# Kernel optimization log

Hardware: AMD Instinct MI355X
Metric: run time of the kernel (lower is better)

The kernel has to match this reference:

```python
import jax, jax.numpy as jnp
import numpy as np

VOCAB, BLOCK, D, H, L = 50257, 2048, 768, 12, 4
B, T = 1, 2048
DH = D // H


def setup_inputs() -> dict:
    key = jax.random.key(0)
    ks = jax.random.split(key, 16)
    s = 0.02
    return {
        "tokens": jax.random.randint(ks[0], (B, T), 0, VOCAB),
        "wte": jax.random.normal(ks[1], (VOCAB, D), jnp.float32) * s,
        "wpe": jax.random.normal(ks[2], (BLOCK, D), jnp.float32) * s,
        "ln1_w": jnp.ones((L, D), jnp.float32),
        "ln1_b": jnp.zeros((L, D), jnp.float32),
        "qkv_w": jax.random.normal(ks[3], (L, D, 3 * D), jnp.float32) * s,
        "qkv_b": jnp.zeros((L, 3 * D), jnp.float32),
        "proj_w": jax.random.normal(ks[4], (L, D, D), jnp.float32) * s,
        "proj_b": jnp.zeros((L, D), jnp.float32),
        "ln2_w": jnp.ones((L, D), jnp.float32),
        "ln2_b": jnp.zeros((L, D), jnp.float32),
        "fc_w": jax.random.normal(ks[5], (L, D, 4 * D), jnp.float32) * s,
        "fc_b": jnp.zeros((L, 4 * D), jnp.float32),
        "fcp_w": jax.random.normal(ks[6], (L, 4 * D, D), jnp.float32) * s,
        "fcp_b": jnp.zeros((L, D), jnp.float32),
        "lnf_w": jnp.ones((D,), jnp.float32),
        "lnf_b": jnp.zeros((D,), jnp.float32),
    }


def _ln(x, w, b, eps=1e-5):
    m = jnp.mean(x, axis=-1, keepdims=True)
    v = jnp.mean((x - m) ** 2, axis=-1, keepdims=True)
    return (x - m) * jax.lax.rsqrt(v + eps) * w + b


def _attn(x, wq, bq, wp, bp):
    Bq, Tq, _ = x.shape
    qkv = x @ wq + bq  # [B,T,3D]
    q, k, v = jnp.split(qkv, 3, axis=-1)
    q = q.reshape(Bq, Tq, H, DH).transpose(0, 2, 1, 3)  # [B,H,T,dh]
    k = k.reshape(Bq, Tq, H, DH).transpose(0, 2, 1, 3)
    v = v.reshape(Bq, Tq, H, DH).transpose(0, 2, 1, 3)
    w = jnp.einsum("bhqd,bhkd->bhqk", q, k) / np.sqrt(DH).astype(np.float32)
    mask = jnp.tril(jnp.ones((Tq, Tq), bool))
    w = jnp.where(mask, w, -jnp.inf)
    w = jax.nn.softmax(w, axis=-1)
    y = jnp.einsum("bhqk,bhkd->bhqd", w, v)
    y = y.transpose(0, 2, 1, 3).reshape(Bq, Tq, D)
    return y @ wp + bp


def reference(tokens, wte, wpe, ln1_w, ln1_b, qkv_w, qkv_b, proj_w, proj_b,
              ln2_w, ln2_b, fc_w, fc_b, fcp_w, fcp_b, lnf_w, lnf_b):
    x = wte[tokens] + wpe[jnp.arange(tokens.shape[1])]  # [B,T,D]
    for l in range(L):
        x = x + _attn(_ln(x, ln1_w[l], ln1_b[l]), qkv_w[l], qkv_b[l], proj_w[l], proj_b[l])
        h = _ln(x, ln2_w[l], ln2_b[l]) @ fc_w[l] + fc_b[l]
        h = jax.nn.gelu(h, approximate=True)
        x = x + h @ fcp_w[l] + fcp_b[l]
    x = _ln(x, lnf_w, lnf_b)
    logits = x @ wte.T  # tied lm_head, [B,T,V]
    return logits
```

## Files before the change

kernel.cpp:

```cpp
#include <hip/hip_runtime.h>
#include <hip/hip_bf16.h>

#define TSEQ   2048
#define DMODEL 768
#define NHEAD  12
#define DHEAD  64
#define NLAYER 4
#define VOCAB  50257
#define VPAD   50304

typedef __attribute__((ext_vector_type(8))) short short8;
typedef __attribute__((ext_vector_type(4))) float f32x4;
typedef unsigned short ushort_t;

union F8 { short8 v; unsigned long long q[2]; };

__device__ __forceinline__ float b2f(ushort_t u) {
  return __uint_as_float(((unsigned)u) << 16);
}
__device__ __forceinline__ ushort_t f2bu(float f) {
  unsigned u = __float_as_uint(f);
  unsigned r = (u + 0x7fffu + ((u >> 16) & 1u)) >> 16;
  return (ushort_t)r;
}

__device__ __forceinline__ void gload_lds16(const void* g, void* l) {
  __builtin_amdgcn_global_load_lds(
      (const __attribute__((address_space(1))) unsigned int*)g,
      (__attribute__((address_space(3))) unsigned int*)l, 16, 0, 0);
}

__global__ __launch_bounds__(256) void embed_kernel(
    const int* __restrict__ tok, const float* __restrict__ wte,
    const float* __restrict__ wpe, float* __restrict__ x) {
  int i = blockIdx.x * 256 + threadIdx.x;
  int t = i / DMODEL;
  int d = i - t * DMODEL;
  x[i] = wte[tok[t] * DMODEL + d] + wpe[i];
}

__global__ __launch_bounds__(256) void cvt_kernel(
    const float* __restrict__ in, ushort_t* __restrict__ out, int n4) {
  for (int i = blockIdx.x * 256 + threadIdx.x; i < n4; i += gridDim.x * 256) {
    float4 f = reinterpret_cast<const float4*>(in)[i];
    ushort4 o;
    o.x = f2bu(f.x); o.y = f2bu(f.y); o.z = f2bu(f.z); o.w = f2bu(f.w);
    reinterpret_cast<ushort4*>(out)[i] = o;
  }
}

__global__ __launch_bounds__(256) void tcvt_kernel(
    const float* __restrict__ W, ushort_t* __restrict__ Wt, int K, int N) {
  __shared__ float Ts[32][33];
  int n0 = blockIdx.x * 32, k0 = blockIdx.y * 32;
  int tx = threadIdx.x & 31, ty = threadIdx.x >> 5;
#pragma unroll
  for (int s = 0; s < 4; ++s)
    Ts[ty + 8 * s][tx] = W[(size_t)(k0 + ty + 8 * s) * N + n0 + tx];
  __syncthreads();
#pragma unroll
  for (int s = 0; s < 4; ++s)
    Wt[(size_t)(n0 + ty + 8 * s) * K + k0 + tx] = f2bu(Ts[tx][ty + 8 * s]);
}

__global__ __launch_bounds__(256) void ln_kernel(
    const float* __restrict__ x, const float* __restrict__ w,
    const float* __restrict__ b, ushort_t* __restrict__ out) {
  int row = blockIdx.x;
  int t = threadIdx.x;
  const float* xr = x + row * DMODEL;
  float v0 = xr[t], v1 = xr[t + 256], v2 = xr[t + 512];
  float s = v0 + v1 + v2;
  float q = v0 * v0 + v1 * v1 + v2 * v2;
#pragma unroll
  for (int off = 32; off >= 1; off >>= 1) {
    s += __shfl_xor(s, off);
    q += __shfl_xor(q, off);
  }
  __shared__ float rs[4], rq[4];
  int wid = t >> 6;
  if ((t & 63) == 0) { rs[wid] = s; rq[wid] = q; }
  __syncthreads();
  s = rs[0] + rs[1] + rs[2] + rs[3];
  q = rq[0] + rq[1] + rq[2] + rq[3];
  float mean = s * (1.f / DMODEL);
  float var  = q * (1.f / DMODEL) - mean * mean;
  float rstd = rsqrtf(var + 1e-5f);
  ushort_t* o = out + row * DMODEL;
  o[t]       = f2bu((v0 - mean) * rstd * w[t]       + b[t]);
  o[t + 256] = f2bu((v1 - mean) * rstd * w[t + 256] + b[t + 256]);
  o[t + 512] = f2bu((v2 - mean) * rstd * w[t + 512] + b[t + 512]);
}

template <int TM, int TN, bool BIAS, bool RES, bool GELU, bool OUTBF16>
__global__ __launch_bounds__(256) void mm_kernel(
    const ushort_t* __restrict__ A, const ushort_t* __restrict__ Bt,
    const float* __restrict__ bias, const float* __restrict__ res,
    void* __restrict__ outp, int N, int K) {
  constexpr int HM = TM / 2, HN = TN / 2, FI = TM / 32, FJ = TN / 32;
  constexpr int NCA = TM / 64, NCB = TN / 64;
  __shared__ ushort_t Asm[TM * 32];
  __shared__ ushort_t Bsm[TN * 32];
  const int tid = threadIdx.x;
  const int lane = tid & 63, wid = tid >> 6;
  const int wr = wid >> 1, wc = wid & 1;
  const int l15 = lane & 15, c4 = lane >> 4;
  const int qc = c4 >> 1, e8 = (c4 & 1) * 8;
  const int rowA0 = blockIdx.y * TM, colB0 = blockIdx.x * TN;

  int aoff[FI], boff[FJ];
#pragma unroll
  for (int i = 0; i < FI; ++i) {
    int r = wr * HM + i * 16 + l15;
    aoff[i] = r * 64 + ((qc ^ ((r >> 1) & 3)) << 4) + e8;
  }
#pragma unroll
  for (int j = 0; j < FJ; ++j) {
    int r = wc * HN + j * 16 + l15;
    boff[j] = r * 64 + ((qc ^ ((r >> 1) & 3)) << 4) + e8;
  }
  const ushort_t* asrc[NCA]; ushort_t* adst[NCA];
  const ushort_t* bsrc[NCB]; ushort_t* bdst[NCB];
#pragma unroll
  for (int s = 0; s < NCA; ++s) {
    int ch = wid + s * 4;
    int r = ch * 16 + (lane >> 2);
    int q = (lane & 3) ^ ((r >> 1) & 3);
    asrc[s] = A + (size_t)(rowA0 + r) * K + q * 8;
    adst[s] = Asm + ch * 512;
  }
#pragma unroll
  for (int s = 0; s < NCB; ++s) {
    int ch = wid + s * 4;
    int r = ch * 16 + (lane >> 2);
    int q = (lane & 3) ^ ((r >> 1) & 3);
    bsrc[s] = Bt + (size_t)(colB0 + r) * K + q * 8;
    bdst[s] = Bsm + ch * 512;
  }

  f32x4 acc[FI][FJ] = {};
  const char* Ab = (const char*)Asm;
  const char* Bb = (const char*)Bsm;

  for (int kt = 0; kt < K; kt += 32) {
    __syncthreads();
#pragma unroll
    for (int s = 0; s < NCA; ++s) gload_lds16(asrc[s] + kt, adst[s]);
#pragma unroll
    for (int s = 0; s < NCB; ++s) gload_lds16(bsrc[s] + kt, bdst[s]);
    __syncthreads();
    short8 a[FI], b[FJ];
#pragma unroll
    for (int i = 0; i < FI; ++i) {
      F8 f;
      f.q[0] = *(const unsigned long long*)(Ab + aoff[i]);
      f.q[1] = *(const unsigned long long*)(Ab + (aoff[i] ^ 32));
      a[i] = f.v;
    }
#pragma unroll
    for (int j = 0; j < FJ; ++j) {
      F8 f;
      f.q[0] = *(const unsigned long long*)(Bb + boff[j]);
      f.q[1] = *(const unsigned long long*)(Bb + (boff[j] ^ 32));
      b[j] = f.v;
    }
#pragma unroll
    for (int i = 0; i < FI; ++i)
#pragma unroll
      for (int j = 0; j < FJ; ++j)
        acc[i][j] = __builtin_amdgcn_mfma_f32_16x16x32_bf16(a[i], b[j], acc[i][j], 0, 0, 0);
  }

#pragma unroll
  for (int i = 0; i < FI; ++i) {
    const int rbase = rowA0 + wr * HM + i * 16 + c4 * 4;
#pragma unroll
    for (int j = 0; j < FJ; ++j) {
      const int col = colB0 + wc * HN + j * 16 + l15;
      if (col < N) {
        float bv = BIAS ? bias[col] : 0.f;
#pragma unroll
        for (int t = 0; t < 4; ++t) {
          float v = acc[i][j][t] + bv;
          if (GELU) {
            float z = 1.5957691216057308f * (v + 0.044715f * v * v * v);
            float th = 1.f - 2.f / (__expf(z) + 1.f);
            v = 0.5f * v * (1.f + th);
          }
          size_t o = (size_t)(rbase + t) * N + col;
          if (RES)          ((float*)outp)[o] = v + res[o];
          else if (OUTBF16) ((ushort_t*)outp)[o] = f2bu(v);
          else              ((float*)outp)[o] = v;
        }
      }
    }
  }
}

__global__ __launch_bounds__(256) void fattn_kernel(
    const ushort_t* __restrict__ qkv, ushort_t* __restrict__ y) {
  const int id = blockIdx.x;
  const int w32 = id / NHEAD;
  const int h = id - w32 * NHEAD;
  const int qb = (w32 & 1) ? (w32 >> 1) : (31 - (w32 >> 1));
  const int q0 = qb * 64;

  __shared__ ushort_t Ksm[64 * 64];
  __shared__ ushort_t Vsm[64 * 64];
  __shared__ ushort_t Psm[4 * 16 * 64];

  const int tid = threadIdx.x;
  const int lane = tid & 63, wv = tid >> 6;
  const int l15 = lane & 15, c4 = lane >> 4;
  const int r7 = l15 & 7;

  const ushort_t* qrow = qkv + (size_t)(q0 + wv * 16 + l15) * (3 * DMODEL) + h * DHEAD;
  const short8 qf0 = *(const short8*)(qrow + c4 * 8);
  const short8 qf1 = *(const short8*)(qrow + 32 + c4 * 8);

  const ushort_t* ksrc[2]; ushort_t* kdst[2];
#pragma unroll
  for (int s = 0; s < 2; ++s) {
    int row = wv * 16 + s * 8 + (lane >> 3);
    int cs = (lane & 7) ^ (row & 7);
    ksrc[s] = qkv + (size_t)row * (3 * DMODEL) + DMODEL + h * DHEAD + cs * 8;
    kdst[s] = Ksm + ((wv * 2 + s) * 64) * 8;
  }
  const int vk = tid & 63, vd0 = (tid >> 6) * 8;
  const ushort_t* vsrc = qkv + (size_t)vk * (3 * DMODEL) + 2 * DMODEL + h * DHEAD;
  const int vkoff = ((vk >> 3) << 3) + (vk & 7);

  float m[4] = {-1e30f, -1e30f, -1e30f, -1e30f};
  float l[4] = {};
  f32x4 acc[4] = {};
  ushort_t* Pw = Psm + wv * 1024;

  for (int k0 = 0; k0 <= q0; k0 += 64) {
    const size_t koff = (size_t)k0 * (3 * DMODEL);
    short8 v0 = *(const short8*)(vsrc + koff + vd0);
    short8 v1 = *(const short8*)(vsrc + koff + vd0 + 32);
    __syncthreads();
#pragma unroll
    for (int s = 0; s < 2; ++s) gload_lds16(ksrc[s] + koff, kdst[s]);
#pragma unroll
    for (int j = 0; j < 8; ++j) {
      int d = vd0 + j;
      Vsm[d * 64 + (vkoff ^ ((d & 7) << 3))] = (ushort_t)v0[j];
      int d2 = d + 32;
      Vsm[d2 * 64 + (vkoff ^ ((d2 & 7) << 3))] = (ushort_t)v1[j];
    }
    __syncthreads();

    f32x4 sv[4];
#pragma unroll
    for (int kt = 0; kt < 4; ++kt) {
      const ushort_t* krow = Ksm + (kt * 16 + l15) * 64;
      short8 kb0 = *(const short8*)(krow + ((c4 ^ r7) << 3));
      short8 kb1 = *(const short8*)(krow + (((4 + c4) ^ r7) << 3));
      f32x4 s = {};
      s = __builtin_amdgcn_mfma_f32_16x16x32_bf16(qf0, kb0, s, 0, 0, 0);
      s = __builtin_amdgcn_mfma_f32_16x16x32_bf16(qf1, kb1, s, 0, 0, 0);
      sv[kt] = s * 0.125f;
    }
    if (k0 == q0) {
#pragma unroll
      for (int kt = 0; kt < 4; ++kt)
#pragma unroll
        for (int r = 0; r < 4; ++r)
          if (kt * 16 + l15 > wv * 16 + c4 * 4 + r) sv[kt][r] = -1e30f;
    }

#pragma unroll
    for (int r = 0; r < 4; ++r) {
      float mv = fmaxf(fmaxf(sv[0][r], sv[1][r]), fmaxf(sv[2][r], sv[3][r]));
      mv = fmaxf(mv, __shfl_xor(mv, 1));
      mv = fmaxf(mv, __shfl_xor(mv, 2));
      mv = fmaxf(mv, __shfl_xor(mv, 4));
      mv = fmaxf(mv, __shfl_xor(mv, 8));
      float nm = fmaxf(m[r], mv);
      float sc = __expf(m[r] - nm);
      m[r] = nm;
      const int row = c4 * 4 + r;
      float sum = 0.f;
#pragma unroll
      for (int kt = 0; kt < 4; ++kt) {
        float p = __expf(sv[kt][r] - nm);
        sum += p;
        Pw[row * 64 + (((kt * 2 + (l15 >> 3)) ^ (row & 7)) << 3) + (l15 & 7)] = f2bu(p);
      }
      sum += __shfl_xor(sum, 1);
      sum += __shfl_xor(sum, 2);
      sum += __shfl_xor(sum, 4);
      sum += __shfl_xor(sum, 8);
      l[r] = l[r] * sc + sum;
#pragma unroll
      for (int j = 0; j < 4; ++j) acc[j][r] *= sc;
    }

    const ushort_t* prow = Pw + l15 * 64;
    short8 pa0 = *(const short8*)(prow + ((c4 ^ r7) << 3));
    short8 pa1 = *(const short8*)(prow + (((4 + c4) ^ r7) << 3));
#pragma unroll
    for (int j = 0; j < 4; ++j) {
      const ushort_t* vrow = Vsm + (j * 16 + l15) * 64;
      short8 vb0 = *(const short8*)(vrow + ((c4 ^ r7) << 3));
      short8 vb1 = *(const short8*)(vrow + (((4 + c4) ^ r7) << 3));
      acc[j] = __builtin_amdgcn_mfma_f32_16x16x32_bf16(pa0, vb0, acc[j], 0, 0, 0);
      acc[j] = __builtin_amdgcn_mfma_f32_16x16x32_bf16(pa1, vb1, acc[j], 0, 0, 0);
    }
  }

  float inv[4];
#pragma unroll
  for (int r = 0; r < 4; ++r) inv[r] = 1.f / l[r];
#pragma unroll
  for (int j = 0; j < 4; ++j)
#pragma unroll
    for (int r = 0; r < 4; ++r)
      y[(size_t)(q0 + wv * 16 + c4 * 4 + r) * DMODEL + h * DHEAD + j * 16 + l15] =
          f2bu(acc[j][r] * inv[r]);
}

extern "C" void kernel_launch(void* const* d_in, const int* in_sizes, int n_in,
                              void* d_out, int out_size, void* d_ws, size_t ws_size,
                              hipStream_t stream) {
  const int*   tokens = (const int*)d_in[0];
  const float* wte    = (const float*)d_in[1];
  const float* wpe    = (const float*)d_in[2];
  const float* ln1_w  = (const float*)d_in[3];
  const float* ln1_b  = (const float*)d_in[4];
  const float* qkv_w  = (const float*)d_in[5];
  const float* qkv_b  = (const float*)d_in[6];
  const float* proj_w = (const float*)d_in[7];
  const float* proj_b = (const float*)d_in[8];
  const float* ln2_w  = (const float*)d_in[9];
  const float* ln2_b  = (const float*)d_in[10];
  const float* fc_w   = (const float*)d_in[11];
  const float* fc_b   = (const float*)d_in[12];
  const float* fcp_w  = (const float*)d_in[13];
  const float* fcp_b  = (const float*)d_in[14];
  const float* lnf_w  = (const float*)d_in[15];
  const float* lnf_b  = (const float*)d_in[16];
  float* out = (float*)d_out;

  char* p = (char*)d_ws;
  auto alloc = [&](size_t bytes) { char* r = p; p += (bytes + 255) & ~(size_t)255; return r; };
  float*    x     = (float*)alloc((size_t)TSEQ * DMODEL * 4);
  ushort_t* lnb   = (ushort_t*)alloc((size_t)TSEQ * DMODEL * 2);
  ushort_t* buf   = (ushort_t*)alloc((size_t)TSEQ * 4 * DMODEL * 2);
  ushort_t* wteb  = (ushort_t*)alloc((size_t)VPAD * DMODEL * 2);
  ushort_t* qkvwt = (ushort_t*)alloc((size_t)NLAYER * 3 * DMODEL * DMODEL * 2);
  ushort_t* projwt= (ushort_t*)alloc((size_t)NLAYER * DMODEL * DMODEL * 2);
  ushort_t* fcwt  = (ushort_t*)alloc((size_t)NLAYER * 4 * DMODEL * DMODEL * 2);
  ushort_t* fcpwt = (ushort_t*)alloc((size_t)NLAYER * 4 * DMODEL * DMODEL * 2);
  ushort_t* qkvb  = buf;
  ushort_t* yb    = buf + (size_t)TSEQ * 3 * DMODEL;
  ushort_t* hfcb  = buf;

  dim3 b256(256);

  cvt_kernel<<<dim3(4096), b256, 0, stream>>>(wte, wteb, VOCAB * DMODEL / 4);
  for (int l = 0; l < NLAYER; ++l) {
    tcvt_kernel<<<dim3(3 * DMODEL / 32, DMODEL / 32), b256, 0, stream>>>(
        qkv_w + (size_t)l * DMODEL * 3 * DMODEL, qkvwt + (size_t)l * 3 * DMODEL * DMODEL,
        DMODEL, 3 * DMODEL);
    tcvt_kernel<<<dim3(DMODEL / 32, DMODEL / 32), b256, 0, stream>>>(
        proj_w + (size_t)l * DMODEL * DMODEL, projwt + (size_t)l * DMODEL * DMODEL,
        DMODEL, DMODEL);
    tcvt_kernel<<<dim3(4 * DMODEL / 32, DMODEL / 32), b256, 0, stream>>>(
        fc_w + (size_t)l * DMODEL * 4 * DMODEL, fcwt + (size_t)l * 4 * DMODEL * DMODEL,
        DMODEL, 4 * DMODEL);
    tcvt_kernel<<<dim3(DMODEL / 32, 4 * DMODEL / 32), b256, 0, stream>>>(
        fcp_w + (size_t)l * 4 * DMODEL * DMODEL, fcpwt + (size_t)l * DMODEL * 4 * DMODEL,
        4 * DMODEL, DMODEL);
  }

  embed_kernel<<<dim3(TSEQ * DMODEL / 256), b256, 0, stream>>>(tokens, wte, wpe, x);

  for (int l = 0; l < NLAYER; ++l) {
    ln_kernel<<<dim3(TSEQ), b256, 0, stream>>>(x, ln1_w + l * DMODEL, ln1_b + l * DMODEL, lnb);
    mm_kernel<128, 128, true, false, false, true><<<dim3(3 * DMODEL / 128, TSEQ / 128), b256, 0, stream>>>(
        lnb, qkvwt + (size_t)l * 3 * DMODEL * DMODEL, qkv_b + (size_t)l * 3 * DMODEL,
        nullptr, qkvb, 3 * DMODEL, DMODEL);
    fattn_kernel<<<dim3(32 * NHEAD), b256, 0, stream>>>(qkvb, yb);
    mm_kernel<64, 64, true, true, false, false><<<dim3(DMODEL / 64, TSEQ / 64), b256, 0, stream>>>(
        yb, projwt + (size_t)l * DMODEL * DMODEL, proj_b + (size_t)l * DMODEL,
        x, x, DMODEL, DMODEL);
    ln_kernel<<<dim3(TSEQ), b256, 0, stream>>>(x, ln2_w + l * DMODEL, ln2_b + l * DMODEL, lnb);
    mm_kernel<128, 128, true, false, true, true><<<dim3(4 * DMODEL / 128, TSEQ / 128), b256, 0, stream>>>(
        lnb, fcwt + (size_t)l * 4 * DMODEL * DMODEL, fc_b + (size_t)l * 4 * DMODEL,
        nullptr, hfcb, 4 * DMODEL, DMODEL);
    mm_kernel<64, 64, true, true, false, false><<<dim3(DMODEL / 64, TSEQ / 64), b256, 0, stream>>>(
        hfcb, fcpwt + (size_t)l * DMODEL * 4 * DMODEL, fcp_b + (size_t)l * DMODEL,
        x, x, DMODEL, 4 * DMODEL);
  }

  ln_kernel<<<dim3(TSEQ), b256, 0, stream>>>(x, lnf_w, lnf_b, lnb);
  mm_kernel<128, 128, false, false, false, false><<<dim3(VPAD / 128, TSEQ / 128), b256, 0, stream>>>(
      lnb, wteb, nullptr, nullptr, out, VOCAB, DMODEL);
}
```

Before: 1.165 ms.

## Double GEMM K-tile to 64 with XOR LDS swizzle and XCD-aware 1D grid

The bf16 MFMA GEMM now stages 64-wide K slices per iteration instead of 32. It uses an 8-chunk XOR swizzle in LDS and runs two MFMA sub-steps per slice, which halves the number of barrier pairs per K loop. Launches switch to a 1D grid where row blocks vary fastest, so neighbouring workgroups share the same weight tile. The lm_head GEMM also permutes block IDs across the 8 XCDs for L2 locality. Weight transpose-convert launches are batched over layers through a z grid dimension, at the cost of doubled LDS use per block and possibly lower occupancy.

```diff
diff --git a/kernel.cpp b/kernel.cpp
--- a/kernel.cpp
+++ b/kernel.cpp
@@ -50,7 +50,10 @@
 }
 
 __global__ __launch_bounds__(256) void tcvt_kernel(
-    const float* __restrict__ W, ushort_t* __restrict__ Wt, int K, int N) {
+    const float* __restrict__ W, ushort_t* __restrict__ Wt, int K, int N,
+    long long wstride) {
+  W  += (size_t)blockIdx.z * wstride;
+  Wt += (size_t)blockIdx.z * wstride;
   __shared__ float Ts[32][33];
   int n0 = blockIdx.x * 32, k0 = blockIdx.y * 32;
   int tx = threadIdx.x & 31, ty = threadIdx.x >> 5;
@@ -92,83 +95,94 @@
   o[t + 512] = f2bu((v2 - mean) * rstd * w[t + 512] + b[t + 512]);
 }
 
-template <int TM, int TN, bool BIAS, bool RES, bool GELU, bool OUTBF16>
+template <int TM, int TN, bool BIAS, bool RES, bool GELU, bool OUTBF16, bool XSWZ>
 __global__ __launch_bounds__(256) void mm_kernel(
     const ushort_t* __restrict__ A, const ushort_t* __restrict__ Bt,
     const float* __restrict__ bias, const float* __restrict__ res,
-    void* __restrict__ outp, int N, int K) {
+    void* __restrict__ outp, int N, int K, int nrowblk, int nwg) {
   constexpr int HM = TM / 2, HN = TN / 2, FI = TM / 32, FJ = TN / 32;
-  constexpr int NCA = TM / 64, NCB = TN / 64;
-  __shared__ ushort_t Asm[TM * 32];
-  __shared__ ushort_t Bsm[TN * 32];
+  constexpr int NCA = TM / 32, NCB = TN / 32;
+  __shared__ ushort_t Asm[TM * 64];
+  __shared__ ushort_t Bsm[TN * 64];
   const int tid = threadIdx.x;
   const int lane = tid & 63, wid = tid >> 6;
   const int wr = wid >> 1, wc = wid & 1;
   const int l15 = lane & 15, c4 = lane >> 4;
-  const int qc = c4 >> 1, e8 = (c4 & 1) * 8;
-  const int rowA0 = blockIdx.y * TM, colB0 = blockIdx.x * TN;
-
-  int aoff[FI], boff[FJ];
+  const int qb0 = (c4 >> 1) << 4;
+  const int qb1 = qb0 + 32;
+  const int e8 = (c4 & 1) * 8;
+
+  int bid = blockIdx.x;
+  if (XSWZ) { int q = nwg >> 3; bid = (bid & 7) * q + (bid >> 3); }
+  const int rowb = bid % nrowblk, colb = bid / nrowblk;
+  const int rowA0 = rowb * TM, colB0 = colb * TN;
+
+  int ap0[FI], ax[FI], bp0[FJ], bx[FJ];
 #pragma unroll
   for (int i = 0; i < FI; ++i) {
     int r = wr * HM + i * 16 + l15;
-    aoff[i] = r * 64 + ((qc ^ ((r >> 1) & 3)) << 4) + e8;
+    ap0[i] = r * 128 + e8; ax[i] = (r & 7) << 4;
   }
 #pragma unroll
   for (int j = 0; j < FJ; ++j) {
     int r = wc * HN + j * 16 + l15;
-    boff[j] = r * 64 + ((qc ^ ((r >> 1) & 3)) << 4) + e8;
-  }
+    bp0[j] = r * 128 + e8; bx[j] = (r & 7) << 4;
+  }
+
   const ushort_t* asrc[NCA]; ushort_t* adst[NCA];
   const ushort_t* bsrc[NCB]; ushort_t* bdst[NCB];
 #pragma unroll
   for (int s = 0; s < NCA; ++s) {
-    int ch = wid + s * 4;
-    int r = ch * 16 + (lane >> 2);
-    int q = (lane & 3) ^ ((r >> 1) & 3);
-    asrc[s] = A + (size_t)(rowA0 + r) * K + q * 8;
-    adst[s] = Asm + ch * 512;
+    int ci = tid + s * 256;
+    int row = ci >> 3;
+    int logch = (ci & 7) ^ (row & 7);
+    asrc[s] = A + (size_t)(rowA0 + row) * K + logch * 8;
+    adst[s] = Asm + ci * 8;
   }
 #pragma unroll
   for (int s = 0; s < NCB; ++s) {
-    int ch = wid + s * 4;
-    int r = ch * 16 + (lane >> 2);
-    int q = (lane & 3) ^ ((r >> 1) & 3);
-    bsrc[s] = Bt + (size_t)(colB0 + r) * K + q * 8;
-    bdst[s] = Bsm + ch * 512;
+    int ci = tid + s * 256;
+    int row = ci >> 3;
+    int logch = (ci & 7) ^ (row & 7);
+    bsrc[s] = Bt + (size_t)(colB0 + row) * K + logch * 8;
+    bdst[s] = Bsm + ci * 8;
   }
 
   f32x4 acc[FI][FJ] = {};
   const char* Ab = (const char*)Asm;
   const char* Bb = (const char*)Bsm;
 
-  for (int kt = 0; kt < K; kt += 32) {
+  for (int kt = 0; kt < K; kt += 64) {
     __syncthreads();
 #pragma unroll
     for (int s = 0; s < NCA; ++s) gload_lds16(asrc[s] + kt, adst[s]);
 #pragma unroll
     for (int s = 0; s < NCB; ++s) gload_lds16(bsrc[s] + kt, bdst[s]);
     __syncthreads();
-    short8 a[FI], b[FJ];
-#pragma unroll
-    for (int i = 0; i < FI; ++i) {
-      F8 f;
-      f.q[0] = *(const unsigned long long*)(Ab + aoff[i]);
-      f.q[1] = *(const unsigned long long*)(Ab + (aoff[i] ^ 32));
-      a[i] = f.v;
-    }
-#pragma unroll
-    for (int j = 0; j < FJ; ++j) {
-      F8 f;
-      f.q[0] = *(const unsigned long long*)(Bb + boff[j]);
-      f.q[1] = *(const unsigned long long*)(Bb + (boff[j] ^ 32));
-      b[j] = f.v;
-    }
-#pragma unroll
-    for (int i = 0; i < FI; ++i)
-#pragma unroll
-      for (int j = 0; j < FJ; ++j)
-        acc[i][j] = __builtin_amdgcn_mfma_f32_16x16x32_bf16(a[i], b[j], acc[i][j], 0, 0, 0);
+#pragma unroll
+    for (int kk = 0; kk < 2; ++kk) {
+      const int k64 = kk * 64;
+      short8 a[FI], b[FJ];
+#pragma unroll
+      for (int i = 0; i < FI; ++i) {
+        F8 f;
+        f.q[0] = *(const unsigned long long*)(Ab + ap0[i] + ((k64 + qb0) ^ ax[i]));
+        f.q[1] = *(const unsigned long long*)(Ab + ap0[i] + ((k64 + qb1) ^ ax[i]));
+        a[i] = f.v;
+      }
+#pragma unroll
+      for (int j = 0; j < FJ; ++j) {
+        F8 f;
+        f.q[0] = *(const unsigned long long*)(Bb + bp0[j] + ((k64 + qb0) ^ bx[j]));
+        f.q[1] = *(const unsigned long long*)(Bb + bp0[j] + ((k64 + qb1) ^ bx[j]));
+        b[j] = f.v;
+      }
+#pragma unroll
+      for (int i = 0; i < FI; ++i)
+#pragma unroll
+        for (int j = 0; j < FJ; ++j)
+          acc[i][j] = __builtin_amdgcn_mfma_f32_16x16x32_bf16(a[i], b[j], acc[i][j], 0, 0, 0);
+    }
   }
 
 #pragma unroll
@@ -360,42 +374,36 @@
   dim3 b256(256);
 
   cvt_kernel<<<dim3(4096), b256, 0, stream>>>(wte, wteb, VOCAB * DMODEL / 4);
-  for (int l = 0; l < NLAYER; ++l) {
-    tcvt_kernel<<<dim3(3 * DMODEL / 32, DMODEL / 32), b256, 0, stream>>>(
-        qkv_w + (size_t)l * DMODEL * 3 * DMODEL, qkvwt + (size_t)l * 3 * DMODEL * DMODEL,
-        DMODEL, 3 * DMODEL);
-    tcvt_kernel<<<dim3(DMODEL / 32, DMODEL / 32), b256, 0, stream>>>(
-        proj_w + (size_t)l * DMODEL * DMODEL, projwt + (size_t)l * DMODEL * DMODEL,
-        DMODEL, DMODEL);
-    tcvt_kernel<<<dim3(4 * DMODEL / 32, DMODEL / 32), b256, 0, stream>>>(
-        fc_w + (size_t)l * DMODEL * 4 * DMODEL, fcwt + (size_t)l * 4 * DMODEL * DMODEL,
-        DMODEL, 4 * DMODEL);
-    tcvt_kernel<<<dim3(DMODEL / 32, 4 * DMODEL / 32), b256, 0, stream>>>(
-        fcp_w + (size_t)l * 4 * DMODEL * DMODEL, fcpwt + (size_t)l * DMODEL * 4 * DMODEL,
-        4 * DMODEL, DMODEL);
-  }
+  tcvt_kernel<<<dim3(3 * DMODEL / 32, DMODEL / 32, NLAYER), b256, 0, stream>>>(
+      qkv_w, qkvwt, DMODEL, 3 * DMODEL, (long long)3 * DMODEL * DMODEL);
+  tcvt_kernel<<<dim3(DMODEL / 32, DMODEL / 32, NLAYER), b256, 0, stream>>>(
+      proj_w, projwt, DMODEL, DMODEL, (long long)DMODEL * DMODEL);
+  tcvt_kernel<<<dim3(4 * DMODEL / 32, DMODEL / 32, NLAYER), b256, 0, stream>>>(
+      fc_w, fcwt, DMODEL, 4 * DMODEL, (long long)4 * DMODEL * DMODEL);
+  tcvt_kernel<<<dim3(DMODEL / 32, 4 * DMODEL / 32, NLAYER), b256, 0, stream>>>(
+      fcp_w, fcpwt, 4 * DMODEL, DMODEL, (long long)4 * DMODEL * DMODEL);
 
   embed_kernel<<<dim3(TSEQ * DMODEL / 256), b256, 0, stream>>>(tokens, wte, wpe, x);
 
   for (int l = 0; l < NLAYER; ++l) {
     ln_kernel<<<dim3(TSEQ), b256, 0, stream>>>(x, ln1_w + l * DMODEL, ln1_b + l * DMODEL, lnb);
-    mm_kernel<128, 128, true, false, false, true><<<dim3(3 * DMODEL / 128, TSEQ / 128), b256, 0, stream>>>(
+    mm_kernel<128, 128, true, false, false, true, false><<<dim3(18 * 16), b256, 0, stream>>>(
         lnb, qkvwt + (size_t)l * 3 * DMODEL * DMODEL, qkv_b + (size_t)l * 3 * DMODEL,
-        nullptr, qkvb, 3 * DMODEL, DMODEL);
+        nullptr, qkvb, 3 * DMODEL, DMODEL, 16, 288);
     fattn_kernel<<<dim3(32 * NHEAD), b256, 0, stream>>>(qkvb, yb);
-    mm_kernel<64, 64, true, true, false, false><<<dim3(DMODEL / 64, TSEQ / 64), b256, 0, stream>>>(
+    mm_kernel<64, 64, true, true, false, false, false><<<dim3(12 * 32), b256, 0, stream>>>(
         yb, projwt + (size_t)l * DMODEL * DMODEL, proj_b + (size_t)l * DMODEL,
-        x, x, DMODEL, DMODEL);
+        x, x, DMODEL, DMODEL, 32, 384);
     ln_kernel<<<dim3(TSEQ), b256, 0, stream>>>(x, ln2_w + l * DMODEL, ln2_b + l * DMODEL, lnb);
-    mm_kernel<128, 128, true, false, true, true><<<dim3(4 * DMODEL / 128, TSEQ / 128), b256, 0, stream>>>(
+    mm_kernel<128, 128, true, false, true, true, false><<<dim3(24 * 16), b256, 0, stream>>>(
         lnb, fcwt + (size_t)l * 4 * DMODEL * DMODEL, fc_b + (size_t)l * 4 * DMODEL,
-        nullptr, hfcb, 4 * DMODEL, DMODEL);
-    mm_kernel<64, 64, true, true, false, false><<<dim3(DMODEL / 64, TSEQ / 64), b256, 0, stream>>>(
+        nullptr, hfcb, 4 * DMODEL, DMODEL, 16, 384);
+    mm_kernel<64, 64, true, true, false, false, false><<<dim3(12 * 32), b256, 0, stream>>>(
         hfcb, fcpwt + (size_t)l * DMODEL * 4 * DMODEL, fcp_b + (size_t)l * DMODEL,
-        x, x, DMODEL, 4 * DMODEL);
+        x, x, DMODEL, 4 * DMODEL, 32, 384);
   }
 
   ln_kernel<<<dim3(TSEQ), b256, 0, stream>>>(x, lnf_w, lnf_b, lnb);
-  mm_kernel<128, 128, false, false, false, false><<<dim3(VPAD / 128, TSEQ / 128), b256, 0, stream>>>(
-      lnb, wteb, nullptr, nullptr, out, VOCAB, DMODEL);
-}
+  mm_kernel<128, 128, false, false, false, false, true><<<dim3(393 * 16), b256, 0, stream>>>(
+      lnb, wteb, nullptr, nullptr, out, VOCAB, DMODEL, 16, 393 * 16);
+}
```

Result: faster. 1.085 ms (-6.8%).
